# Optimization experiments

Hardware: AMD Instinct MI355X
Metric: run time of the kernel (lower is better)

The kernel has to match this reference:

```python
import jax, jax.numpy as jnp
import numpy as np

N_NODES = 100000
N_EDGES = 1600000
F_IN, F_HID, F_OUT = 64, 64, 32


def _glorot_linear(key, fan_in, fan_out, bias=True):
    # torch.nn.Linear default init: kaiming_uniform on W, uniform on b
    k1, k2 = jax.random.split(key)
    bound_w = 1.0 / np.sqrt(fan_in)
    W = jax.random.uniform(k1, (fan_out, fan_in), minval=-bound_w, maxval=bound_w, dtype=jnp.float32)
    if bias:
        b = jax.random.uniform(k2, (fan_out,), minval=-bound_w, maxval=bound_w, dtype=jnp.float32)
        return W, b
    return W, None


def setup_inputs() -> dict:
    key = jax.random.key(0)
    ks = jax.random.split(key, 8)
    x = jax.random.normal(ks[0], (N_NODES, F_IN), dtype=jnp.float32)
    edge_index = jax.random.randint(ks[1], (2, N_EDGES), 0, N_NODES, dtype=jnp.int64)
    Wl0, bl0 = _glorot_linear(ks[2], F_IN, F_HID, bias=True)
    Wr0, _ = _glorot_linear(ks[3], F_IN, F_HID, bias=False)
    Wl1, bl1 = _glorot_linear(ks[4], F_HID, F_OUT, bias=True)
    Wr1, _ = _glorot_linear(ks[5], F_HID, F_OUT, bias=False)
    return {"x": x, "edge_index": edge_index,
            "Wl0": Wl0, "bl0": bl0, "Wr0": Wr0,
            "Wl1": Wl1, "bl1": bl1, "Wr1": Wr1}


def _sage_conv(x, edge_index, Wl, bl, Wr):
    # out = mean-aggregate(lin_l(x)[src] -> dst) + lin_r(x)
    h = x @ Wl.T + bl                      # [N, out]
    src, dst = edge_index[0], edge_index[1]
    msgs = h[src]                          # [E, out] gather (irregular)
    summed = jax.ops.segment_sum(msgs, dst, num_segments=x.shape[0])
    cnt = jax.ops.segment_sum(jnp.ones_like(dst, dtype=h.dtype), dst,
                              num_segments=x.shape[0])
    agg = summed / jnp.maximum(cnt, 1.0)[:, None]  # scatter-mean; isolated nodes -> 0
    return agg + x @ Wr.T


def reference(x, edge_index, Wl0, bl0, Wr0, Wl1, bl1, Wr1):
    # GNN.forward with num_layers=2, conv='sage', eval-mode dropout (identity).
    h = jax.nn.relu(_sage_conv(x, edge_index, Wl0, bl0, Wr0))
    out = _sage_conv(h, edge_index, Wl1, bl1, Wr1)
    return out
```

## Files before the change

kernel.cpp:

```cpp
#include <hip/hip_runtime.h>

#define N_NODES 100000
#define N_EDGES 1600000
#define NWIN 1024
#define WN 98
#define WCAP 2048
#define PB ((N_EDGES + 4095) / 4096)
#define NTILES ((N_NODES + 63) / 64)

typedef __attribute__((ext_vector_type(8))) short bf16x8;
typedef __attribute__((ext_vector_type(4))) float f32x4;

__device__ __forceinline__ unsigned short f2bf(float f) {
  unsigned u = __builtin_bit_cast(unsigned, f);
  u += 0x7FFFu + ((u >> 16) & 1u);
  return (unsigned short)(u >> 16);
}
__device__ __forceinline__ float bf2f(unsigned short s) {
  return __builtin_bit_cast(float, (unsigned)s << 16);
}

__global__ __launch_bounds__(256) void conv_bf16(
    const float4* __restrict__ X4, const float4* __restrict__ Wr0,
    const float4* __restrict__ Wl0, const float4* __restrict__ Wl1,
    const float4* __restrict__ Wr1, ushort4* __restrict__ Xb,
    ushort4* __restrict__ Wb) {
  const int i = blockIdx.x * 256 + threadIdx.x;
  float4 v;
  ushort4* dst;
  if (i < N_NODES * 16) {
    v = X4[i];
    dst = &Xb[i];
  } else {
    const int j = i - N_NODES * 16;
    if (j < 1024) v = Wr0[j];
    else if (j < 2048) v = Wl0[j - 1024];
    else if (j < 2560) v = Wl1[j - 2048];
    else if (j < 3072) v = Wr1[j - 2560];
    else return;
    dst = &Wb[j];
  }
  ushort4 o;
  o.x = f2bf(v.x); o.y = f2bf(v.y); o.z = f2bf(v.z); o.w = f2bf(v.w);
  *dst = o;
}

__global__ __launch_bounds__(256) void part_hist(const int* __restrict__ ei,
                                                 unsigned short* __restrict__ bh) {
  __shared__ unsigned h[NWIN];
  const int t = threadIdx.x;
  for (int i = t; i < NWIN; i += 256) h[i] = 0;
  __syncthreads();
  const int base = blockIdx.x * 4096;
#pragma unroll
  for (int i = 0; i < 16; ++i) {
    const int e = base + i * 256 + t;
    if (e < N_EDGES) {
      const unsigned d = (unsigned)ei[N_EDGES + e];
      atomicAdd(&h[d / WN], 1u);
    }
  }
  __syncthreads();
  for (int i = t; i < NWIN; i += 256)
    bh[(size_t)blockIdx.x * NWIN + i] = (unsigned short)h[i];
}

__global__ __launch_bounds__(64) void col_scan(
    const unsigned short* __restrict__ bh, unsigned short* __restrict__ boff,
    unsigned* __restrict__ colsum) {
  const int w = blockIdx.x;
  const int lane = threadIdx.x;
  unsigned run = 0;
#pragma unroll
  for (int j = 0; j < 7; ++j) {
    const int b = j * 64 + lane;
    const unsigned v = (b < PB) ? (unsigned)bh[(size_t)b * NWIN + w] : 0u;
    unsigned sc = v;
#pragma unroll
    for (int off = 1; off < 64; off <<= 1) {
      const unsigned u = __shfl_up(sc, off, 64);
      if (lane >= off) sc += u;
    }
    if (b < PB) boff[(size_t)b * NWIN + w] = (unsigned short)(run + sc - v);
    run += __shfl(sc, 63, 64);
  }
  if (lane == 0) colsum[w] = run;
}

__global__ __launch_bounds__(1024) void base_scan(
    const unsigned* __restrict__ colsum, unsigned* __restrict__ bbase) {
  __shared__ unsigned s[NWIN];
  const int t = threadIdx.x;
  const unsigned v = colsum[t];
  s[t] = v;
  __syncthreads();
  for (int off = 1; off < NWIN; off <<= 1) {
    const unsigned u = (t >= off) ? s[t - off] : 0u;
    __syncthreads();
    s[t] += u;
    __syncthreads();
  }
  bbase[t] = s[t] - v;
}

__global__ __launch_bounds__(256) void part_fill(const int* __restrict__ ei,
                                                 const unsigned short* __restrict__ boff,
                                                 const unsigned* __restrict__ bbase,
                                                 unsigned* __restrict__ ebuf) {
  __shared__ unsigned cur[NWIN];
  const int t = threadIdx.x;
  for (int i = t; i < NWIN; i += 256)
    cur[i] = bbase[i] + (unsigned)boff[(size_t)blockIdx.x * NWIN + i];
  __syncthreads();
  const int base = blockIdx.x * 4096;
#pragma unroll
  for (int i = 0; i < 16; ++i) {
    const int e = base + i * 256 + t;
    if (e < N_EDGES) {
      const unsigned s = (unsigned)ei[e];
      const unsigned d = (unsigned)ei[N_EDGES + e];
      const unsigned b = d / WN, dl = d - b * WN;
      const unsigned pos = atomicAdd(&cur[b], 1u);
      ebuf[pos] = (dl << 24) | s;
    }
  }
}

__global__ __launch_bounds__(256) void win_sort(unsigned* __restrict__ ebuf,
                                                const unsigned* __restrict__ colsum,
                                                const unsigned* __restrict__ bbase,
                                                unsigned* __restrict__ rowptr,
                                                unsigned* __restrict__ deg) {
  __shared__ unsigned earr[WCAP];
  __shared__ unsigned sorted[WCAP];
  __shared__ unsigned hist[WN], pre[WN], cur[WN];
  const int t = threadIdx.x, w = blockIdx.x;
  const int lo = w * WN;
  const unsigned sbase = bbase[w];
  const int n = min((int)colsum[w], WCAP);
  for (int i = t; i < WN; i += 256) hist[i] = 0;
  __syncthreads();
  for (int i = t; i < n; i += 256) {
    const unsigned p = ebuf[sbase + i];
    earr[i] = p;
    atomicAdd(&hist[p >> 24], 1u);
  }
  __syncthreads();
  if (t == 0) {
    unsigned run = 0;
    for (int i = 0; i < WN; ++i) {
      pre[i] = run;
      run += hist[i];
    }
  }
  __syncthreads();
  for (int dl = t; dl < WN; dl += 256) {
    const int node = lo + dl;
    if (node < N_NODES) {
      rowptr[node] = sbase + pre[dl];
      deg[node] = hist[dl];
    }
    cur[dl] = pre[dl];
  }
  __syncthreads();
  for (int i = t; i < n; i += 256) {
    const unsigned p = earr[i];
    const unsigned pos = atomicAdd(&cur[p >> 24], 1u);
    sorted[pos] = p;
  }
  __syncthreads();
  for (int i = t; i < n; i += 256) ebuf[sbase + i] = sorted[i];
}

__global__ __launch_bounds__(256) void gemm01_mfma(
    const unsigned short* __restrict__ Xb,
    const unsigned short* __restrict__ AGGb,
    const unsigned short* __restrict__ Wb, const float* __restrict__ bl0,
    const unsigned* __restrict__ deg, const float* __restrict__ bl1,
    unsigned short* __restrict__ H1b, float* __restrict__ HR1) {
  __shared__ unsigned short sH[64 * 72];
  const int t = threadIdx.x;
  const int lane = t & 63;
  const int w = t >> 6;
  const int rbase = blockIdx.x * 64;
  const int lr = lane & 15;
  const int kg = lane >> 4;
  const int row16 = w * 16 + lr;
  const int grow_a = rbase + row16;
  const size_t arow = (size_t)(grow_a < N_NODES ? grow_a : N_NODES - 1);

  const unsigned short* Wr0b = Wb;
  const unsigned short* Wl0b = Wb + 4096;
  const unsigned short* Wl1b = Wb + 8192;
  const unsigned short* Wr1b = Wb + 10240;

  f32x4 acc[4] = {{0, 0, 0, 0}, {0, 0, 0, 0}, {0, 0, 0, 0}, {0, 0, 0, 0}};

  {
    const bf16x8 ax0 = *(const bf16x8*)&Xb[arow * 64 + kg * 8];
    const bf16x8 ax1 = *(const bf16x8*)&Xb[arow * 64 + 32 + kg * 8];
    const bf16x8 ag0 = *(const bf16x8*)&AGGb[arow * 64 + kg * 8];
    const bf16x8 ag1 = *(const bf16x8*)&AGGb[arow * 64 + 32 + kg * 8];
#pragma unroll
    for (int cn = 0; cn < 4; ++cn) {
      const int wr = cn * 16 + lr;
      const bf16x8 br0 = *(const bf16x8*)&Wr0b[wr * 64 + kg * 8];
      const bf16x8 br1 = *(const bf16x8*)&Wr0b[wr * 64 + 32 + kg * 8];
      const bf16x8 bl0f = *(const bf16x8*)&Wl0b[wr * 64 + kg * 8];
      const bf16x8 bl1f = *(const bf16x8*)&Wl0b[wr * 64 + 32 + kg * 8];
      acc[cn] = __builtin_amdgcn_mfma_f32_16x16x32_bf16(ax0, br0, acc[cn], 0, 0, 0);
      acc[cn] = __builtin_amdgcn_mfma_f32_16x16x32_bf16(ax1, br1, acc[cn], 0, 0, 0);
      acc[cn] = __builtin_amdgcn_mfma_f32_16x16x32_bf16(ag0, bl0f, acc[cn], 0, 0, 0);
      acc[cn] = __builtin_amdgcn_mfma_f32_16x16x32_bf16(ag1, bl1f, acc[cn], 0, 0, 0);
    }
  }

  const int crow0 = w * 16 + (lane >> 4) * 4;
  float gate[4];
#pragma unroll
  for (int r = 0; r < 4; ++r) {
    const int grow = rbase + crow0 + r;
    gate[r] = (deg[grow < N_NODES ? grow : N_NODES - 1] > 0) ? 1.0f : 0.0f;
  }
#pragma unroll
  for (int cn = 0; cn < 4; ++cn) {
    const int col = cn * 16 + lr;
    const float bias = bl0[col];
#pragma unroll
    for (int r = 0; r < 4; ++r) {
      const float h = fmaxf(fmaf(bias, gate[r], acc[cn][r]), 0.0f);
      sH[(crow0 + r) * 72 + col] = f2bf(h);
    }
  }
  __syncthreads();

  f32x4 acc2[4] = {{0, 0, 0, 0}, {0, 0, 0, 0}, {0, 0, 0, 0}, {0, 0, 0, 0}};
  {
    const bf16x8 ah0 = *(const bf16x8*)&sH[row16 * 72 + kg * 8];
    const bf16x8 ah1 = *(const bf16x8*)&sH[row16 * 72 + 32 + kg * 8];
#pragma unroll
    for (int cn = 0; cn < 4; ++cn) {
      const int col = cn * 16 + lr;
      const unsigned short* Wp =
          (cn < 2) ? &Wl1b[col * 64] : &Wr1b[(col - 32) * 64];
      const bf16x8 b0 = *(const bf16x8*)&Wp[kg * 8];
      const bf16x8 b1 = *(const bf16x8*)&Wp[32 + kg * 8];
      acc2[cn] = __builtin_amdgcn_mfma_f32_16x16x32_bf16(ah0, b0, acc2[cn], 0, 0, 0);
      acc2[cn] = __builtin_amdgcn_mfma_f32_16x16x32_bf16(ah1, b1, acc2[cn], 0, 0, 0);
    }
  }

#pragma unroll
  for (int cn = 0; cn < 4; ++cn) {
    const int col = cn * 16 + lr;
    const float bias = (cn < 2) ? bl1[col] : 0.0f;
#pragma unroll
    for (int r = 0; r < 4; ++r) {
      const int grow = rbase + crow0 + r;
      if (grow < N_NODES) {
        if (cn < 2)
          H1b[(size_t)grow * 32 + col] = f2bf(acc2[cn][r] + bias);
        else
          HR1[(size_t)grow * 32 + (col - 32)] = acc2[cn][r];
      }
    }
  }
}

__global__ __launch_bounds__(256) void gather64_bf16(
    const ushort4* __restrict__ Xb, const unsigned* __restrict__ rowptr,
    const unsigned* __restrict__ degp, const unsigned* __restrict__ csr,
    ushort4* __restrict__ aggxb) {
  const int node = (int)((blockIdx.x * 256 + threadIdx.x) >> 6);
  const int lane = threadIdx.x & 63;
  if (node >= N_NODES) return;
  const int g = lane >> 4, q = lane & 15;
  const unsigned beg = rowptr[node];
  const unsigned d = degp[node];
  const unsigned end = beg + d;
  const float inv = d ? 1.0f / (float)d : 0.0f;

  float ax = 0, ay = 0, az = 0, aw = 0, bx = 0, by = 0, bz = 0, bw = 0;
  unsigned e = beg + g;
  for (; e + 4 < end; e += 8) {
    const ushort4 u0 = Xb[(size_t)(csr[e] & 0xFFFFFFu) * 16 + q];
    const ushort4 u1 = Xb[(size_t)(csr[e + 4] & 0xFFFFFFu) * 16 + q];
    ax += bf2f(u0.x); ay += bf2f(u0.y); az += bf2f(u0.z); aw += bf2f(u0.w);
    bx += bf2f(u1.x); by += bf2f(u1.y); bz += bf2f(u1.z); bw += bf2f(u1.w);
  }
  if (e < end) {
    const ushort4 u = Xb[(size_t)(csr[e] & 0xFFFFFFu) * 16 + q];
    ax += bf2f(u.x); ay += bf2f(u.y); az += bf2f(u.z); aw += bf2f(u.w);
  }
  float sx = ax + bx, sy = ay + by, sz = az + bz, sw = aw + bw;
#pragma unroll
  for (int m = 16; m < 64; m <<= 1) {
    sx += __shfl_xor(sx, m, 64);
    sy += __shfl_xor(sy, m, 64);
    sz += __shfl_xor(sz, m, 64);
    sw += __shfl_xor(sw, m, 64);
  }
  if (g == 0) {
    ushort4 o;
    o.x = f2bf(sx * inv); o.y = f2bf(sy * inv);
    o.z = f2bf(sz * inv); o.w = f2bf(sw * inv);
    aggxb[(size_t)node * 16 + q] = o;
  }
}

__global__ __launch_bounds__(256) void gather32_bf16(
    const ushort4* __restrict__ H1b, const unsigned* __restrict__ rowptr,
    const unsigned* __restrict__ degp, const unsigned* __restrict__ csr,
    const float4* __restrict__ HR1, float4* __restrict__ outp) {
  const int node = (int)((blockIdx.x * 256 + threadIdx.x) >> 6);
  const int lane = threadIdx.x & 63;
  if (node >= N_NODES) return;
  const int g = lane >> 3, q = lane & 7;
  const unsigned beg = rowptr[node];
  const unsigned d = degp[node];
  const unsigned end = beg + d;
  const float inv = d ? 1.0f / (float)d : 0.0f;

  float ax = 0, ay = 0, az = 0, aw = 0, bx = 0, by = 0, bz = 0, bw = 0;
  unsigned e = beg + g;
  for (; e + 8 < end; e += 16) {
    const ushort4 u0 = H1b[(size_t)(csr[e] & 0xFFFFFFu) * 8 + q];
    const ushort4 u1 = H1b[(size_t)(csr[e + 8] & 0xFFFFFFu) * 8 + q];
    ax += bf2f(u0.x); ay += bf2f(u0.y); az += bf2f(u0.z); aw += bf2f(u0.w);
    bx += bf2f(u1.x); by += bf2f(u1.y); bz += bf2f(u1.z); bw += bf2f(u1.w);
  }
  if (e < end) {
    const ushort4 u = H1b[(size_t)(csr[e] & 0xFFFFFFu) * 8 + q];
    ax += bf2f(u.x); ay += bf2f(u.y); az += bf2f(u.z); aw += bf2f(u.w);
  }
  float sx = ax + bx, sy = ay + by, sz = az + bz, sw = aw + bw;
#pragma unroll
  for (int m = 8; m < 64; m <<= 1) {
    sx += __shfl_xor(sx, m, 64);
    sy += __shfl_xor(sy, m, 64);
    sz += __shfl_xor(sz, m, 64);
    sw += __shfl_xor(sw, m, 64);
  }
  if (g == 0) {
    const float4 b = HR1[(size_t)node * 8 + q];
    float4 r;
    r.x = sx * inv + b.x;
    r.y = sy * inv + b.y;
    r.z = sz * inv + b.z;
    r.w = sw * inv + b.w;
    outp[(size_t)node * 8 + q] = r;
  }
}

extern "C" void kernel_launch(void* const* d_in, const int* in_sizes, int n_in,
                              void* d_out, int out_size, void* d_ws,
                              size_t ws_size, hipStream_t stream) {
  const float* x = (const float*)d_in[0];
  const int* ei = (const int*)d_in[1];
  const float* Wl0 = (const float*)d_in[2];
  const float* bl0 = (const float*)d_in[3];
  const float* Wr0 = (const float*)d_in[4];
  const float* Wl1 = (const float*)d_in[5];
  const float* bl1 = (const float*)d_in[6];
  const float* Wr1 = (const float*)d_in[7];
  float* out = (float*)d_out;

  const int N = N_NODES;

  unsigned short* xb = (unsigned short*)d_ws;
  unsigned short* aggxb = xb + (size_t)N * 64;
  unsigned short* h1b = aggxb + (size_t)N * 64;
  unsigned short* Wb = h1b + (size_t)N * 32;
  float* hr1 = (float*)(Wb + 12288);
  unsigned* deg = (unsigned*)(hr1 + (size_t)N * 32);
  unsigned* rowptr = deg + N;
  unsigned* colsum = rowptr + N;
  unsigned* bbase = colsum + NWIN;
  unsigned short* bh = (unsigned short*)(bbase + NWIN);
  unsigned short* boff = bh + (size_t)PB * NWIN;
  unsigned* ebuf = (unsigned*)(boff + (size_t)PB * NWIN);

  const dim3 blk(256);

  conv_bf16<<<(N * 16 + 3072 + 255) / 256, blk, 0, stream>>>(
      (const float4*)x, (const float4*)Wr0, (const float4*)Wl0,
      (const float4*)Wl1, (const float4*)Wr1, (ushort4*)xb, (ushort4*)Wb);

  part_hist<<<PB, blk, 0, stream>>>(ei, bh);
  col_scan<<<NWIN, 64, 0, stream>>>(bh, boff, colsum);
  base_scan<<<1, NWIN, 0, stream>>>(colsum, bbase);
  part_fill<<<PB, blk, 0, stream>>>(ei, boff, bbase, ebuf);
  win_sort<<<NWIN, blk, 0, stream>>>(ebuf, colsum, bbase, rowptr, deg);

  gather64_bf16<<<(N * 64 + 255) / 256, blk, 0, stream>>>(
      (const ushort4*)xb, rowptr, deg, ebuf, (ushort4*)aggxb);

  gemm01_mfma<<<NTILES, blk, 0, stream>>>(xb, aggxb, Wb, bl0, deg, bl1, h1b,
                                          hr1);

  gather32_bf16<<<(N * 64 + 255) / 256, blk, 0, stream>>>(
      (const ushort4*)h1b, rowptr, deg, ebuf, (const float4*)hr1,
      (float4*)out);
}
```

Baseline: 165.3 us.

## Fuse layer-0 neighbor gather into MFMA GEMM and use power-of-two windows

The separate gather64 kernel is removed. Each GEMM block now computes the mean aggregation for its 64 nodes straight into shared memory, and that tile feeds the MFMA, so the bf16 aggregate buffer is no longer written to or read from global memory. Destination windows change to 64 nodes so the partition can use shifts instead of division, and the window count is aligned with the GEMM tiles. The base scan becomes a single-wave shuffle scan. The trade-off is parallelism: each wave now walks 16 nodes one after another instead of one wave per node, which may hurt the latency hiding of the irregular gathers.

```diff
diff --git a/kernel.cpp b/kernel.cpp
--- a/kernel.cpp
+++ b/kernel.cpp
@@ -2,11 +2,11 @@
 
 #define N_NODES 100000
 #define N_EDGES 1600000
-#define NWIN 1024
-#define WN 98
-#define WCAP 2048
+#define NWIN 1563
+#define WN 64
+#define WCAP 1536
 #define PB ((N_EDGES + 4095) / 4096)
-#define NTILES ((N_NODES + 63) / 64)
+#define NTILES NWIN
 
 typedef __attribute__((ext_vector_type(8))) short bf16x8;
 typedef __attribute__((ext_vector_type(4))) float f32x4;
@@ -57,7 +57,7 @@
     const int e = base + i * 256 + t;
     if (e < N_EDGES) {
       const unsigned d = (unsigned)ei[N_EDGES + e];
-      atomicAdd(&h[d / WN], 1u);
+      atomicAdd(&h[d >> 6], 1u);
     }
   }
   __syncthreads();
@@ -72,7 +72,7 @@
   const int lane = threadIdx.x;
   unsigned run = 0;
 #pragma unroll
-  for (int j = 0; j < 7; ++j) {
+  for (int j = 0; j < (PB + 63) / 64; ++j) {
     const int b = j * 64 + lane;
     const unsigned v = (b < PB) ? (unsigned)bh[(size_t)b * NWIN + w] : 0u;
     unsigned sc = v;
@@ -87,20 +87,22 @@
   if (lane == 0) colsum[w] = run;
 }
 
-__global__ __launch_bounds__(1024) void base_scan(
+__global__ __launch_bounds__(64) void base_scan(
     const unsigned* __restrict__ colsum, unsigned* __restrict__ bbase) {
-  __shared__ unsigned s[NWIN];
-  const int t = threadIdx.x;
-  const unsigned v = colsum[t];
-  s[t] = v;
-  __syncthreads();
-  for (int off = 1; off < NWIN; off <<= 1) {
-    const unsigned u = (t >= off) ? s[t - off] : 0u;
-    __syncthreads();
-    s[t] += u;
-    __syncthreads();
-  }
-  bbase[t] = s[t] - v;
+  const int lane = threadIdx.x;
+  unsigned run = 0;
+  for (int j = 0; j < (NWIN + 63) / 64; ++j) {
+    const int w = j * 64 + lane;
+    const unsigned v = (w < NWIN) ? colsum[w] : 0u;
+    unsigned sc = v;
+#pragma unroll
+    for (int off = 1; off < 64; off <<= 1) {
+      const unsigned u = __shfl_up(sc, off, 64);
+      if (lane >= off) sc += u;
+    }
+    if (w < NWIN) bbase[w] = run + sc - v;
+    run += __shfl(sc, 63, 64);
+  }
 }
 
 __global__ __launch_bounds__(256) void part_fill(const int* __restrict__ ei,
@@ -119,9 +121,8 @@
     if (e < N_EDGES) {
       const unsigned s = (unsigned)ei[e];
       const unsigned d = (unsigned)ei[N_EDGES + e];
-      const unsigned b = d / WN, dl = d - b * WN;
-      const unsigned pos = atomicAdd(&cur[b], 1u);
-      ebuf[pos] = (dl << 24) | s;
+      const unsigned pos = atomicAdd(&cur[d >> 6], 1u);
+      ebuf[pos] = ((d & 63u) << 24) | s;
     }
   }
 }
@@ -138,7 +139,7 @@
   const int lo = w * WN;
   const unsigned sbase = bbase[w];
   const int n = min((int)colsum[w], WCAP);
-  for (int i = t; i < WN; i += 256) hist[i] = 0;
+  if (t < WN) hist[t] = 0;
   __syncthreads();
   for (int i = t; i < n; i += 256) {
     const unsigned p = ebuf[sbase + i];
@@ -154,13 +155,13 @@
     }
   }
   __syncthreads();
-  for (int dl = t; dl < WN; dl += 256) {
-    const int node = lo + dl;
+  if (t < WN) {
+    const int node = lo + t;
     if (node < N_NODES) {
-      rowptr[node] = sbase + pre[dl];
-      deg[node] = hist[dl];
-    }
-    cur[dl] = pre[dl];
+      rowptr[node] = sbase + pre[t];
+      deg[node] = hist[t];
+    }
+    cur[t] = pre[t];
   }
   __syncthreads();
   for (int i = t; i < n; i += 256) {
@@ -172,17 +173,59 @@
   for (int i = t; i < n; i += 256) ebuf[sbase + i] = sorted[i];
 }
 
-__global__ __launch_bounds__(256) void gemm01_mfma(
-    const unsigned short* __restrict__ Xb,
-    const unsigned short* __restrict__ AGGb,
+__global__ __launch_bounds__(256) void gather_gemm(
+    const unsigned short* __restrict__ Xb, const unsigned* __restrict__ rowptr,
+    const unsigned* __restrict__ degp, const unsigned* __restrict__ csr,
     const unsigned short* __restrict__ Wb, const float* __restrict__ bl0,
-    const unsigned* __restrict__ deg, const float* __restrict__ bl1,
-    unsigned short* __restrict__ H1b, float* __restrict__ HR1) {
-  __shared__ unsigned short sH[64 * 72];
+    const float* __restrict__ bl1, unsigned short* __restrict__ H1b,
+    float* __restrict__ HR1) {
+  __shared__ unsigned short sT[64 * 72];
   const int t = threadIdx.x;
   const int lane = t & 63;
   const int w = t >> 6;
   const int rbase = blockIdx.x * 64;
+  const ushort4* __restrict__ X4 = (const ushort4*)Xb;
+
+  {
+    const int g = lane >> 4, q = lane & 15;
+    for (int nl = 0; nl < 16; ++nl) {
+      const int node = rbase + w * 16 + nl;
+      float ax = 0, ay = 0, az = 0, aw_ = 0, bx = 0, by = 0, bz = 0, bw = 0;
+      unsigned d = 0;
+      if (node < N_NODES) {
+        const unsigned beg = rowptr[node];
+        d = degp[node];
+        const unsigned end = beg + d;
+        unsigned e = beg + g;
+        for (; e + 4 < end; e += 8) {
+          const ushort4 u0 = X4[(size_t)(csr[e] & 0xFFFFFFu) * 16 + q];
+          const ushort4 u1 = X4[(size_t)(csr[e + 4] & 0xFFFFFFu) * 16 + q];
+          ax += bf2f(u0.x); ay += bf2f(u0.y); az += bf2f(u0.z); aw_ += bf2f(u0.w);
+          bx += bf2f(u1.x); by += bf2f(u1.y); bz += bf2f(u1.z); bw += bf2f(u1.w);
+        }
+        if (e < end) {
+          const ushort4 u = X4[(size_t)(csr[e] & 0xFFFFFFu) * 16 + q];
+          ax += bf2f(u.x); ay += bf2f(u.y); az += bf2f(u.z); aw_ += bf2f(u.w);
+        }
+      }
+      float sx = ax + bx, sy = ay + by, sz = az + bz, sw = aw_ + bw;
+#pragma unroll
+      for (int m = 16; m < 64; m <<= 1) {
+        sx += __shfl_xor(sx, m, 64);
+        sy += __shfl_xor(sy, m, 64);
+        sz += __shfl_xor(sz, m, 64);
+        sw += __shfl_xor(sw, m, 64);
+      }
+      if (g == 0) {
+        const float inv = d ? 1.0f / (float)d : 0.0f;
+        ushort4 o;
+        o.x = f2bf(sx * inv); o.y = f2bf(sy * inv);
+        o.z = f2bf(sz * inv); o.w = f2bf(sw * inv);
+        *(ushort4*)&sT[(w * 16 + nl) * 72 + q * 4] = o;
+      }
+    }
+  }
+
   const int lr = lane & 15;
   const int kg = lane >> 4;
   const int row16 = w * 16 + lr;
@@ -199,8 +242,8 @@
   {
     const bf16x8 ax0 = *(const bf16x8*)&Xb[arow * 64 + kg * 8];
     const bf16x8 ax1 = *(const bf16x8*)&Xb[arow * 64 + 32 + kg * 8];
-    const bf16x8 ag0 = *(const bf16x8*)&AGGb[arow * 64 + kg * 8];
-    const bf16x8 ag1 = *(const bf16x8*)&AGGb[arow * 64 + 32 + kg * 8];
+    const bf16x8 ag0 = *(const bf16x8*)&sT[row16 * 72 + kg * 8];
+    const bf16x8 ag1 = *(const bf16x8*)&sT[row16 * 72 + 32 + kg * 8];
 #pragma unroll
     for (int cn = 0; cn < 4; ++cn) {
       const int wr = cn * 16 + lr;
@@ -220,7 +263,7 @@
 #pragma unroll
   for (int r = 0; r < 4; ++r) {
     const int grow = rbase + crow0 + r;
-    gate[r] = (deg[grow < N_NODES ? grow : N_NODES - 1] > 0) ? 1.0f : 0.0f;
+    gate[r] = (degp[grow < N_NODES ? grow : N_NODES - 1] > 0) ? 1.0f : 0.0f;
   }
 #pragma unroll
   for (int cn = 0; cn < 4; ++cn) {
@@ -229,15 +272,14 @@
 #pragma unroll
     for (int r = 0; r < 4; ++r) {
       const float h = fmaxf(fmaf(bias, gate[r], acc[cn][r]), 0.0f);
-      sH[(crow0 + r) * 72 + col] = f2bf(h);
-    }
-  }
-  __syncthreads();
+      sT[(crow0 + r) * 72 + col] = f2bf(h);
+    }
+  }
 
   f32x4 acc2[4] = {{0, 0, 0, 0}, {0, 0, 0, 0}, {0, 0, 0, 0}, {0, 0, 0, 0}};
   {
-    const bf16x8 ah0 = *(const bf16x8*)&sH[row16 * 72 + kg * 8];
-    const bf16x8 ah1 = *(const bf16x8*)&sH[row16 * 72 + 32 + kg * 8];
+    const bf16x8 ah0 = *(const bf16x8*)&sT[row16 * 72 + kg * 8];
+    const bf16x8 ah1 = *(const bf16x8*)&sT[row16 * 72 + 32 + kg * 8];
 #pragma unroll
     for (int cn = 0; cn < 4; ++cn) {
       const int col = cn * 16 + lr;
@@ -264,47 +306,6 @@
           HR1[(size_t)grow * 32 + (col - 32)] = acc2[cn][r];
       }
     }
-  }
-}
-
-__global__ __launch_bounds__(256) void gather64_bf16(
-    const ushort4* __restrict__ Xb, const unsigned* __restrict__ rowptr,
-    const unsigned* __restrict__ degp, const unsigned* __restrict__ csr,
-    ushort4* __restrict__ aggxb) {
-  const int node = (int)((blockIdx.x * 256 + threadIdx.x) >> 6);
-  const int lane = threadIdx.x & 63;
-  if (node >= N_NODES) return;
-  const int g = lane >> 4, q = lane & 15;
-  const unsigned beg = rowptr[node];
-  const unsigned d = degp[node];
-  const unsigned end = beg + d;
-  const float inv = d ? 1.0f / (float)d : 0.0f;
-
-  float ax = 0, ay = 0, az = 0, aw = 0, bx = 0, by = 0, bz = 0, bw = 0;
-  unsigned e = beg + g;
-  for (; e + 4 < end; e += 8) {
-    const ushort4 u0 = Xb[(size_t)(csr[e] & 0xFFFFFFu) * 16 + q];
-    const ushort4 u1 = Xb[(size_t)(csr[e + 4] & 0xFFFFFFu) * 16 + q];
-    ax += bf2f(u0.x); ay += bf2f(u0.y); az += bf2f(u0.z); aw += bf2f(u0.w);
-    bx += bf2f(u1.x); by += bf2f(u1.y); bz += bf2f(u1.z); bw += bf2f(u1.w);
-  }
-  if (e < end) {
-    const ushort4 u = Xb[(size_t)(csr[e] & 0xFFFFFFu) * 16 + q];
-    ax += bf2f(u.x); ay += bf2f(u.y); az += bf2f(u.z); aw += bf2f(u.w);
-  }
-  float sx = ax + bx, sy = ay + by, sz = az + bz, sw = aw + bw;
-#pragma unroll
-  for (int m = 16; m < 64; m <<= 1) {
-    sx += __shfl_xor(sx, m, 64);
-    sy += __shfl_xor(sy, m, 64);
-    sz += __shfl_xor(sz, m, 64);
-    sw += __shfl_xor(sw, m, 64);
-  }
-  if (g == 0) {
-    ushort4 o;
-    o.x = f2bf(sx * inv); o.y = f2bf(sy * inv);
-    o.z = f2bf(sz * inv); o.w = f2bf(sw * inv);
-    aggxb[(size_t)node * 16 + q] = o;
   }
 }
 
@@ -368,8 +369,7 @@
   const int N = N_NODES;
 
   unsigned short* xb = (unsigned short*)d_ws;
-  unsigned short* aggxb = xb + (size_t)N * 64;
-  unsigned short* h1b = aggxb + (size_t)N * 64;
+  unsigned short* h1b = xb + (size_t)N * 64;
   unsigned short* Wb = h1b + (size_t)N * 32;
   float* hr1 = (float*)(Wb + 12288);
   unsigned* deg = (unsigned*)(hr1 + (size_t)N * 32);
@@ -378,7 +378,7 @@
   unsigned* bbase = colsum + NWIN;
   unsigned short* bh = (unsigned short*)(bbase + NWIN);
   unsigned short* boff = bh + (size_t)PB * NWIN;
-  unsigned* ebuf = (unsigned*)(boff + (size_t)PB * NWIN);
+  unsigned* ebuf = (unsigned*)(boff + (size_t)PB * NWIN + 2 );
 
   const dim3 blk(256);
 
@@ -388,15 +388,12 @@
 
   part_hist<<<PB, blk, 0, stream>>>(ei, bh);
   col_scan<<<NWIN, 64, 0, stream>>>(bh, boff, colsum);
-  base_scan<<<1, NWIN, 0, stream>>>(colsum, bbase);
+  base_scan<<<1, 64, 0, stream>>>(colsum, bbase);
   part_fill<<<PB, blk, 0, stream>>>(ei, boff, bbase, ebuf);
   win_sort<<<NWIN, blk, 0, stream>>>(ebuf, colsum, bbase, rowptr, deg);
 
-  gather64_bf16<<<(N * 64 + 255) / 256, blk, 0, stream>>>(
-      (const ushort4*)xb, rowptr, deg, ebuf, (ushort4*)aggxb);
-
-  gemm01_mfma<<<NTILES, blk, 0, stream>>>(xb, aggxb, Wb, bl0, deg, bl1, h1b,
-                                          hr1);
+  gather_gemm<<<NTILES, blk, 0, stream>>>(xb, rowptr, deg, ebuf, Wb, bl0, bl1,
+                                          h1b, hr1);
 
   gather32_bf16<<<(N * 64 + 255) / 256, blk, 0, stream>>>(
       (const ushort4*)h1b, rowptr, deg, ebuf, (const float4*)hr1,
```

New measurement: 207.3 us. 1.25x slower.
